# Optimization experiments

Hardware: AMD Instinct MI355X
Metric: run time of the kernel (lower is better)

Reference implementation:

```python
import jax, jax.numpy as jnp
import numpy as np

EMBED_DIM = 128
B, SQ, SKV = 16, 2048, 2048


def setup_inputs() -> dict:
    key = jax.random.key(0)
    ks = jax.random.split(key, 8)
    d = EMBED_DIM
    scale = 1.0 / np.sqrt(d)
    return {
        "x": jax.random.normal(ks[0], (B, SQ, d), dtype=jnp.float32),
        "y": jax.random.normal(ks[1], (B, SKV, d), dtype=jnp.float32),
        "Wq": jax.random.normal(ks[2], (d, d), dtype=jnp.float32) * scale,
        "bq": jax.random.normal(ks[3], (d,), dtype=jnp.float32) * 0.02,
        "Wk": jax.random.normal(ks[4], (d, d), dtype=jnp.float32) * scale,
        "bk": jax.random.normal(ks[5], (d,), dtype=jnp.float32) * 0.02,
        "Wv": jax.random.normal(ks[6], (d, d), dtype=jnp.float32) * scale,
        "bv": jax.random.normal(ks[7], (d,), dtype=jnp.float32) * 0.02,
    }


def reference(x, y, Wq, bq, Wk, bk, Wv, bv):
    # Linear projections (torch Linear: x @ W.T + b; here W stored as [in,out])
    q = x @ Wq + bq            # [B, SQ, d]
    k = y @ Wk + bk            # [B, SKV, d]
    v = y @ Wv + bv            # [B, SKV, d]
    # Source scales by q.size(-1)**0.5 = sqrt(embed_dim)
    inv_scale = 1.0 / jnp.sqrt(jnp.asarray(q.shape[-1], q.dtype))
    scores = jnp.einsum("bqd,bkd->bqk", q, k) * inv_scale  # [B, SQ, SKV]
    attn = jax.nn.softmax(scores, axis=-1)
    return jnp.einsum("bqk,bkd->bqd", attn, v)
```

## Files before the change

kernel.cpp:

```cpp
#include <hip/hip_runtime.h>
#include <hip/hip_bf16.h>

typedef unsigned short ushort_t;
typedef __attribute__((ext_vector_type(8))) short short8;
typedef __attribute__((ext_vector_type(4))) float f32x4;
typedef __attribute__((ext_vector_type(16))) float f32x16;

#define MFMA16(a, b, c) __builtin_amdgcn_mfma_f32_16x16x32_bf16((a), (b), (c), 0, 0, 0)
#define MFMA32(a, b, c) __builtin_amdgcn_mfma_f32_32x32x16_bf16((a), (b), (c), 0, 0, 0)

__device__ __forceinline__ ushort_t f2bf(float f) {
    return __builtin_bit_cast(ushort_t, __float2bfloat16(f));
}

#define CVTPK(lo, hi) ({ unsigned int r_; \
    asm("v_cvt_pk_bf16_f32 %0, %1, %2" : "=v"(r_) : "v"(lo), "v"(hi)); r_; })

__device__ __forceinline__ void gl_lds16(const void* g, void* l) {
    __builtin_amdgcn_global_load_lds((const __attribute__((address_space(1))) void*)g,
                                     (__attribute__((address_space(3))) void*)l, 16, 0, 0);
}

__global__ __launch_bounds__(256) void wt_kernel(
    const float* __restrict__ Wq, const float* __restrict__ Wk, const float* __restrict__ Wv,
    ushort_t* __restrict__ WTq, ushort_t* __restrict__ WTk, ushort_t* __restrict__ WTv)
{
    __shared__ __align__(16) ushort_t wt2[128 * 24];

    const int mat  = blockIdx.x >> 3;
    const int slab = blockIdx.x & 7;
    const float* W = (mat == 0) ? Wq : (mat == 1) ? Wk : Wv;
    ushort_t*   WT = (mat == 0) ? WTq : (mat == 1) ? WTk : WTv;

    const int t = threadIdx.x;
    #pragma unroll
    for (int i = 0; i < 2; ++i) {
        int idx = t + i * 256;
        int kloc = idx >> 5;
        int c0   = (idx & 31) * 4;
        f32x4 v = ((const f32x4*)(W + (size_t)(slab * 16) * 128))[idx];
        #pragma unroll
        for (int j = 0; j < 4; ++j)
            wt2[(c0 + j) * 24 + kloc] = f2bf(v[j]);
    }
    __syncthreads();
    const int r    = t >> 1;
    const int half = t & 1;
    short8 v8 = *(const short8*)&wt2[r * 24 + half * 8];
    *(short8*)(WT + r * 128 + slab * 16 + half * 8) = v8;
}

__global__ __launch_bounds__(256) void proj_kernel(
    const float* __restrict__ src, const ushort_t* __restrict__ WT,
    const float* __restrict__ bias, ushort_t* __restrict__ dst, float scale)
{
    const int t = threadIdx.x;
    const int w  = t >> 6;
    const int l  = t & 63;
    const int lg = l >> 4;
    const int ln = l & 15;
    const int r0 = blockIdx.x * 64 + w * 16;
    const int acol = lg * 8;

    short8 afrag[4];
    #pragma unroll
    for (int kc = 0; kc < 4; ++kc) {
        const f32x4* p = (const f32x4*)(src + (size_t)(r0 + ln) * 128 + acol + kc * 32);
        f32x4 a0 = p[0], a1 = p[1];
        short8 a;
        #pragma unroll
        for (int j = 0; j < 4; ++j) { a[j] = (short)f2bf(a0[j]); a[4 + j] = (short)f2bf(a1[j]); }
        afrag[kc] = a;
    }

    #pragma unroll
    for (int ct = 0; ct < 8; ++ct) {
        f32x4 acc = {0.f, 0.f, 0.f, 0.f};
        const int c = ct * 16 + ln;
        #pragma unroll
        for (int kc = 0; kc < 4; ++kc) {
            short8 bfr = *(const short8*)(WT + c * 128 + kc * 32 + acol);
            acc = MFMA16(afrag[kc], bfr, acc);
        }
        float bv = bias[c];
        #pragma unroll
        for (int reg = 0; reg < 4; ++reg) {
            int row = r0 + lg * 4 + reg;
            dst[(size_t)row * 128 + c] = f2bf((acc[reg] + bv) * scale);
        }
    }
}

__global__ __launch_bounds__(256) void projKV_kernel(
    const float* __restrict__ src,
    const ushort_t* __restrict__ WTk, const float* __restrict__ bk,
    const ushort_t* __restrict__ WTv, const float* __restrict__ bv,
    ushort_t* __restrict__ Kd, ushort_t* __restrict__ VTd)
{
    __shared__ __align__(16) ushort_t vt[128 * 64];

    const int t = threadIdx.x;
    const int w  = t >> 6;
    const int l  = t & 63;
    const int lg = l >> 4;
    const int ln = l & 15;
    const int r0 = blockIdx.x * 64 + w * 16;
    const int acol = lg * 8;

    short8 afrag[4];
    #pragma unroll
    for (int kc = 0; kc < 4; ++kc) {
        const f32x4* p = (const f32x4*)(src + (size_t)(r0 + ln) * 128 + acol + kc * 32);
        f32x4 a0 = p[0], a1 = p[1];
        short8 a;
        #pragma unroll
        for (int j = 0; j < 4; ++j) { a[j] = (short)f2bf(a0[j]); a[4 + j] = (short)f2bf(a1[j]); }
        afrag[kc] = a;
    }

    #pragma unroll
    for (int ct = 0; ct < 8; ++ct) {
        f32x4 acc = {0.f, 0.f, 0.f, 0.f};
        const int c = ct * 16 + ln;
        #pragma unroll
        for (int kc = 0; kc < 4; ++kc) {
            short8 bfr = *(const short8*)(WTk + c * 128 + kc * 32 + acol);
            acc = MFMA16(afrag[kc], bfr, acc);
        }
        float bvv = bk[c];
        #pragma unroll
        for (int reg = 0; reg < 4; ++reg) {
            int row = r0 + lg * 4 + reg;
            Kd[(size_t)row * 128 + c] = f2bf(acc[reg] + bvv);
        }
    }

    #pragma unroll
    for (int ct = 0; ct < 8; ++ct) {
        f32x4 acc = {0.f, 0.f, 0.f, 0.f};
        const int c = ct * 16 + ln;
        #pragma unroll
        for (int kc = 0; kc < 4; ++kc) {
            short8 bfr = *(const short8*)(WTv + c * 128 + kc * 32 + acol);
            acc = MFMA16(afrag[kc], bfr, acc);
        }
        float bvv = bv[c];
        #pragma unroll
        for (int reg = 0; reg < 4; ++reg) {
            int rloc = w * 16 + lg * 4 + reg;
            int byte = (c * 128 + rloc * 2) ^ ((c & 7) << 4);
            *(ushort_t*)((char*)vt + byte) = f2bf(acc[reg] + bvv);
        }
    }
    __syncthreads();

    const int r0b = blockIdx.x * 64;
    const int b   = r0b >> 11;
    const int kv0 = r0b & 2047;
    const int c    = t >> 1;
    const int half = t & 1;
    ushort_t* dst = VTd + (size_t)b * 128 * 2048 + (size_t)c * 2048 + kv0 + half * 32;
    #pragma unroll
    for (int j = 0; j < 4; ++j) {
        int byte = (c * 128 + (half * 32 + j * 8) * 2) ^ ((c & 7) << 4);
        *(short8*)(dst + j * 8) = *(const short8*)((const char*)vt + byte);
    }
}

#define KVBLK 64
#define NT (2048 / KVBLK)
__global__ __launch_bounds__(256) void attn_kernel(
    const ushort_t* __restrict__ Q, const ushort_t* __restrict__ K,
    const ushort_t* __restrict__ VT, float* __restrict__ out)
{
    __shared__ __align__(16) char smem_[65536];

    const int t = threadIdx.x;
    const int bid = (int)blockIdx.x;
    const int wg = (bid & 7) * 64 + (bid >> 3);
    const int b  = wg >> 5;
    const int q0blk = (wg & 31) * 64;

    const char* Kb  = (const char*)(K  + (size_t)b * 2048 * 128);
    const char* VTb = (const char*)(VT + (size_t)b * 128 * 2048);
    const ushort_t* Qb = Q + (size_t)b * 2048 * 128;

    const int w   = t >> 6;
    const int qg  = w >> 1;
    const int kvh = w & 1;
    const int l  = t & 63;
    const int lq = l & 31;
    const int h  = l >> 5;
    const int swz = (l & 7) << 4;
    const int q0 = q0blk + qg * 32;

    short8 qfrag[8];
    {
        const ushort_t* qp = Qb + (size_t)(q0 + lq) * 128 + h * 8;
        #pragma unroll
        for (int kc = 0; kc < 8; ++kc)
            qfrag[kc] = *(const short8*)(qp + kc * 16);
    }

    f32x16 o[4];
    #pragma unroll
    for (int db = 0; db < 4; ++db)
        #pragma unroll
        for (int i = 0; i < 16; ++i) o[db][i] = 0.f;
    float m = -__builtin_inff(), lsum = 0.f;

    auto stage = [&](int buf, int kt) {
        const char* kb = Kb + (size_t)kt * KVBLK * 256;
        const int kv2 = kt * KVBLK * 2;
        char* kd = smem_ + buf * 16384;
        char* vd = smem_ + 32768 + buf * 16384;
        #pragma unroll
        for (int i = 0; i < 4; ++i) {
            int base = w * 4096 + i * 1024;
            int p = base + l * 16;
            int spk = p ^ (((p >> 8) & 7) << 4);
            gl_lds16(kb + spk, kd + base);
            int spv = p ^ (((p >> 7) & 7) << 4);
            gl_lds16(VTb + (size_t)(spv >> 7) * 4096 + kv2 + (spv & 127), vd + base);
        }
    };

    stage(0, 0);
    int cur = 0;

    for (int kt = 0; kt < NT; ++kt) {
        __syncthreads();
        if (kt + 1 < NT) stage(cur ^ 1, kt + 1);

        const char* klp = smem_ + cur * 16384;
        f32x16 s;
        #pragma unroll
        for (int i = 0; i < 16; ++i) s[i] = 0.f;
        const int krow = kvh * 32 + lq;
        __builtin_amdgcn_s_setprio(1);
        #pragma unroll
        for (int kc = 0; kc < 8; ++kc) {
            int col = (h * 16 + kc * 32) ^ swz;
            short8 kf = *(const short8*)(klp + krow * 256 + col);
            s = MFMA32(kf, qfrag[kc], s);
        }
        __builtin_amdgcn_s_setprio(0);

        float mx;
        {
            float t8[8];
            #pragma unroll
            for (int i = 0; i < 8; ++i) t8[i] = fmaxf(s[i], s[i + 8]);
            #pragma unroll
            for (int i = 0; i < 4; ++i) t8[i] = fmaxf(t8[i], t8[i + 4]);
            mx = fmaxf(fmaxf(t8[0], t8[1]), fmaxf(t8[2], t8[3]));
        }
        mx = fmaxf(mx, __shfl_xor(mx, 32));

        if (__any(mx > m + 8.f)) {
            float mn = fmaxf(m, mx);
            float corr = __builtin_exp2f(m - mn);
            lsum *= corr;
            #pragma unroll
            for (int db = 0; db < 4; ++db)
                #pragma unroll
                for (int i = 0; i < 16; ++i) o[db][i] *= corr;
            m = mn;
        }
        #pragma unroll
        for (int i = 0; i < 16; ++i) s[i] = __builtin_exp2f(s[i] - m);
        float rs;
        {
            float a8[8];
            #pragma unroll
            for (int i = 0; i < 8; ++i) a8[i] = s[i] + s[i + 8];
            #pragma unroll
            for (int i = 0; i < 4; ++i) a8[i] += a8[i + 4];
            rs = (a8[0] + a8[1]) + (a8[2] + a8[3]);
        }
        rs += __shfl_xor(rs, 32);
        lsum += rs;

        short8 pf[2];
        {
            auto pack = [&](int a, short8& outf) {
                unsigned u0 = CVTPK(s[a * 8 + 0], s[a * 8 + 1]);
                unsigned u1 = CVTPK(s[a * 8 + 2], s[a * 8 + 3]);
                unsigned u2 = CVTPK(s[a * 8 + 4], s[a * 8 + 5]);
                unsigned u3 = CVTPK(s[a * 8 + 6], s[a * 8 + 7]);
                unsigned x0 = __shfl_xor(u0, 32);
                unsigned x1 = __shfl_xor(u1, 32);
                unsigned x2 = __shfl_xor(u2, 32);
                unsigned x3 = __shfl_xor(u3, 32);
                union { unsigned wds[4]; short8 s8; } f;
                f.wds[0] = h ? x2 : u0;
                f.wds[1] = h ? x3 : u1;
                f.wds[2] = h ? u2 : x0;
                f.wds[3] = h ? u3 : x1;
                outf = f.s8;
            };
            pack(0, pf[0]);
            pack(1, pf[1]);
        }

        const char* vlp = smem_ + 32768 + cur * 16384;
        __builtin_amdgcn_s_setprio(1);
        #pragma unroll
        for (int db = 0; db < 4; ++db) {
            int row = db * 32 + lq;
            #pragma unroll
            for (int ks = 0; ks < 2; ++ks) {
                int byte = row * 128 + ((kvh * 64 + ks * 32 + h * 16) ^ swz);
                short8 vf = *(const short8*)(vlp + byte);
                o[db] = MFMA32(vf, pf[ks], o[db]);
            }
        }
        __builtin_amdgcn_s_setprio(0);
        cur ^= 1;
    }

    __syncthreads();
    float* mrg = (float*)smem_;
    const int mo = qg * 4224 + lq * 132;
    const int mlb = 8448;

    if (kvh == 1) {
        #pragma unroll
        for (int db = 0; db < 4; ++db) {
            #pragma unroll
            for (int rq = 0; rq < 4; ++rq) {
                f32x4 v4;
                #pragma unroll
                for (int j = 0; j < 4; ++j) v4[j] = o[db][rq * 4 + j];
                *(f32x4*)&mrg[mo + db * 32 + rq * 8 + 4 * h] = v4;
            }
        }
        if (h == 0) {
            mrg[mlb + qg * 64 + lq] = m;
            mrg[mlb + 128 + qg * 64 + lq] = lsum;
        }
    }
    __syncthreads();
    if (kvh == 0) {
        float mB = mrg[mlb + qg * 64 + lq];
        float lB = mrg[mlb + 128 + qg * 64 + lq];
        float mF = fmaxf(m, mB);
        float cA = __builtin_exp2f(m - mF);
        float cB = __builtin_exp2f(mB - mF);
        float inv = 1.0f / (lsum * cA + lB * cB);
        float* ob = out + (size_t)b * 2048 * 128 + (size_t)(q0 + lq) * 128;
        #pragma unroll
        for (int db = 0; db < 4; ++db) {
            #pragma unroll
            for (int rq = 0; rq < 4; ++rq) {
                f32x4 p4 = *(const f32x4*)&mrg[mo + db * 32 + rq * 8 + 4 * h];
                f32x4 st;
                #pragma unroll
                for (int j = 0; j < 4; ++j)
                    st[j] = (o[db][rq * 4 + j] * cA + p4[j] * cB) * inv;
                *(f32x4*)(ob + db * 32 + rq * 8 + 4 * h) = st;
            }
        }
    }
}

extern "C" void kernel_launch(void* const* d_in, const int* in_sizes, int n_in,
                              void* d_out, int out_size, void* d_ws, size_t ws_size,
                              hipStream_t stream) {
    (void)in_sizes; (void)n_in; (void)out_size; (void)ws_size;
    const float* x  = (const float*)d_in[0];
    const float* y  = (const float*)d_in[1];
    const float* Wq = (const float*)d_in[2];
    const float* bq = (const float*)d_in[3];
    const float* Wk = (const float*)d_in[4];
    const float* bk = (const float*)d_in[5];
    const float* Wv = (const float*)d_in[6];
    const float* bv = (const float*)d_in[7];
    float* out = (float*)d_out;

    ushort_t* wtq = (ushort_t*)d_out;
    ushort_t* wtk = wtq + 16384;
    ushort_t* wtv = wtk + 16384;

    ushort_t* qws  = (ushort_t*)d_ws;
    ushort_t* kws  = qws + (size_t)32768 * 128;
    ushort_t* vtws = kws + (size_t)32768 * 128;

    const float qscale = (float)(1.4426950408889634 / 11.313708498984761);

    wt_kernel<<<24, 256, 0, stream>>>(Wq, Wk, Wv, wtq, wtk, wtv);
    proj_kernel<<<512, 256, 0, stream>>>(x, wtq, bq, qws, qscale);
    projKV_kernel<<<512, 256, 0, stream>>>(y, wtk, bk, wtv, bv, kws, vtws);
    attn_kernel<<<512, 256, 0, stream>>>(qws, kws, vtws, out);
}
```

Measured before the change: 103.4 us.

## Merge projection kernels and restructure attention to split KV across four waves

Q and KV projections are merged into one launch, and the Q/K outputs are staged through an LDS tile so global stores are coalesced. The attention kernel drops LDS double-buffered K/V staging in favour of direct global loads into registers. Each block now handles 32 queries, with the four waves splitting the KV range and combining their partial softmax states in a tree merge through LDS. Launch bounds request three blocks per CU. The aim is more parallelism and lower LDS pressure, at the cost of uncoalesced, unshared global K/V reads that rely on L2 and are repeated per block.

```diff
diff --git a/kernel.cpp b/kernel.cpp
--- a/kernel.cpp
+++ b/kernel.cpp
@@ -15,11 +15,6 @@
 
 #define CVTPK(lo, hi) ({ unsigned int r_; \
     asm("v_cvt_pk_bf16_f32 %0, %1, %2" : "=v"(r_) : "v"(lo), "v"(hi)); r_; })
-
-__device__ __forceinline__ void gl_lds16(const void* g, void* l) {
-    __builtin_amdgcn_global_load_lds((const __attribute__((address_space(1))) void*)g,
-                                     (__attribute__((address_space(3))) void*)l, 16, 0, 0);
-}
 
 __global__ __launch_bounds__(256) void wt_kernel(
     const float* __restrict__ Wq, const float* __restrict__ Wk, const float* __restrict__ Wv,
@@ -50,16 +45,27 @@
     *(short8*)(WT + r * 128 + slab * 16 + half * 8) = v8;
 }
 
-__global__ __launch_bounds__(256) void proj_kernel(
-    const float* __restrict__ src, const ushort_t* __restrict__ WT,
-    const float* __restrict__ bias, ushort_t* __restrict__ dst, float scale)
+__global__ __launch_bounds__(256) void proj_all(
+    const float* __restrict__ x, const float* __restrict__ y,
+    const ushort_t* __restrict__ WTq, const float* __restrict__ bq,
+    const ushort_t* __restrict__ WTk, const float* __restrict__ bk,
+    const ushort_t* __restrict__ WTv, const float* __restrict__ bv,
+    ushort_t* __restrict__ Qd, ushort_t* __restrict__ Kd, ushort_t* __restrict__ VTd,
+    float qscale)
 {
+    __shared__ __align__(16) ushort_t tile[64][140];
+    __shared__ __align__(16) ushort_t vt[128 * 64];
+
     const int t = threadIdx.x;
+    const bool isQ = blockIdx.x < 512;
+    const int pb = isQ ? blockIdx.x : (blockIdx.x - 512);
+    const float* src = isQ ? x : y;
+
     const int w  = t >> 6;
     const int l  = t & 63;
     const int lg = l >> 4;
     const int ln = l & 15;
-    const int r0 = blockIdx.x * 64 + w * 16;
+    const int r0 = pb * 64 + w * 16;
     const int acol = lg * 8;
 
     short8 afrag[4];
@@ -73,126 +79,89 @@
         afrag[kc] = a;
     }
 
+    const ushort_t* WT1 = isQ ? WTq : WTk;
+    const float*    b1  = isQ ? bq  : bk;
+    const float     sc  = isQ ? qscale : 1.0f;
+
     #pragma unroll
     for (int ct = 0; ct < 8; ++ct) {
         f32x4 acc = {0.f, 0.f, 0.f, 0.f};
         const int c = ct * 16 + ln;
         #pragma unroll
         for (int kc = 0; kc < 4; ++kc) {
-            short8 bfr = *(const short8*)(WT + c * 128 + kc * 32 + acol);
+            short8 bfr = *(const short8*)(WT1 + c * 128 + kc * 32 + acol);
             acc = MFMA16(afrag[kc], bfr, acc);
         }
-        float bv = bias[c];
-        #pragma unroll
-        for (int reg = 0; reg < 4; ++reg) {
-            int row = r0 + lg * 4 + reg;
-            dst[(size_t)row * 128 + c] = f2bf((acc[reg] + bv) * scale);
-        }
-    }
-}
-
-__global__ __launch_bounds__(256) void projKV_kernel(
-    const float* __restrict__ src,
-    const ushort_t* __restrict__ WTk, const float* __restrict__ bk,
-    const ushort_t* __restrict__ WTv, const float* __restrict__ bv,
-    ushort_t* __restrict__ Kd, ushort_t* __restrict__ VTd)
-{
-    __shared__ __align__(16) ushort_t vt[128 * 64];
-
-    const int t = threadIdx.x;
-    const int w  = t >> 6;
-    const int l  = t & 63;
-    const int lg = l >> 4;
-    const int ln = l & 15;
-    const int r0 = blockIdx.x * 64 + w * 16;
-    const int acol = lg * 8;
-
-    short8 afrag[4];
-    #pragma unroll
-    for (int kc = 0; kc < 4; ++kc) {
-        const f32x4* p = (const f32x4*)(src + (size_t)(r0 + ln) * 128 + acol + kc * 32);
-        f32x4 a0 = p[0], a1 = p[1];
-        short8 a;
-        #pragma unroll
-        for (int j = 0; j < 4; ++j) { a[j] = (short)f2bf(a0[j]); a[4 + j] = (short)f2bf(a1[j]); }
-        afrag[kc] = a;
-    }
-
-    #pragma unroll
-    for (int ct = 0; ct < 8; ++ct) {
-        f32x4 acc = {0.f, 0.f, 0.f, 0.f};
-        const int c = ct * 16 + ln;
-        #pragma unroll
-        for (int kc = 0; kc < 4; ++kc) {
-            short8 bfr = *(const short8*)(WTk + c * 128 + kc * 32 + acol);
-            acc = MFMA16(afrag[kc], bfr, acc);
-        }
-        float bvv = bk[c];
-        #pragma unroll
-        for (int reg = 0; reg < 4; ++reg) {
-            int row = r0 + lg * 4 + reg;
-            Kd[(size_t)row * 128 + c] = f2bf(acc[reg] + bvv);
-        }
-    }
-
-    #pragma unroll
-    for (int ct = 0; ct < 8; ++ct) {
-        f32x4 acc = {0.f, 0.f, 0.f, 0.f};
-        const int c = ct * 16 + ln;
-        #pragma unroll
-        for (int kc = 0; kc < 4; ++kc) {
-            short8 bfr = *(const short8*)(WTv + c * 128 + kc * 32 + acol);
-            acc = MFMA16(afrag[kc], bfr, acc);
-        }
-        float bvv = bv[c];
-        #pragma unroll
-        for (int reg = 0; reg < 4; ++reg) {
-            int rloc = w * 16 + lg * 4 + reg;
-            int byte = (c * 128 + rloc * 2) ^ ((c & 7) << 4);
-            *(ushort_t*)((char*)vt + byte) = f2bf(acc[reg] + bvv);
-        }
-    }
-    __syncthreads();
-
-    const int r0b = blockIdx.x * 64;
-    const int b   = r0b >> 11;
-    const int kv0 = r0b & 2047;
-    const int c    = t >> 1;
-    const int half = t & 1;
-    ushort_t* dst = VTd + (size_t)b * 128 * 2048 + (size_t)c * 2048 + kv0 + half * 32;
-    #pragma unroll
-    for (int j = 0; j < 4; ++j) {
-        int byte = (c * 128 + (half * 32 + j * 8) * 2) ^ ((c & 7) << 4);
-        *(short8*)(dst + j * 8) = *(const short8*)((const char*)vt + byte);
-    }
-}
-
-#define KVBLK 64
-#define NT (2048 / KVBLK)
-__global__ __launch_bounds__(256) void attn_kernel(
+        float bvv = b1[c];
+        #pragma unroll
+        for (int reg = 0; reg < 4; ++reg)
+            tile[w * 16 + lg * 4 + reg][c] = f2bf((acc[reg] + bvv) * sc);
+    }
+
+    if (!isQ) {
+        #pragma unroll
+        for (int ct = 0; ct < 8; ++ct) {
+            f32x4 acc = {0.f, 0.f, 0.f, 0.f};
+            const int c = ct * 16 + ln;
+            #pragma unroll
+            for (int kc = 0; kc < 4; ++kc) {
+                short8 bfr = *(const short8*)(WTv + c * 128 + kc * 32 + acol);
+                acc = MFMA16(afrag[kc], bfr, acc);
+            }
+            float bvv = bv[c];
+            #pragma unroll
+            for (int reg = 0; reg < 4; ++reg) {
+                int rloc = w * 16 + lg * 4 + reg;
+                int byte = (c * 128 + rloc * 2) ^ ((c & 7) << 4);
+                *(ushort_t*)((char*)vt + byte) = f2bf(acc[reg] + bvv);
+            }
+        }
+    }
+    __syncthreads();
+
+    {
+        const int row = t >> 2, ch = t & 3;
+        ushort_t* dst1 = (isQ ? Qd : Kd) + (size_t)(pb * 64 + row) * 128 + ch * 32;
+        #pragma unroll
+        for (int j = 0; j < 4; ++j)
+            *(short8*)(dst1 + j * 8) = *(const short8*)&tile[row][ch * 32 + j * 8];
+    }
+    if (!isQ) {
+        const int r0b = pb * 64;
+        const int b   = r0b >> 11;
+        const int kv0 = r0b & 2047;
+        const int c    = t >> 1;
+        const int half = t & 1;
+        ushort_t* dst = VTd + (size_t)b * 128 * 2048 + (size_t)c * 2048 + kv0 + half * 32;
+        #pragma unroll
+        for (int j = 0; j < 4; ++j) {
+            int byte = (c * 128 + (half * 32 + j * 8) * 2) ^ ((c & 7) << 4);
+            *(short8*)(dst + j * 8) = *(const short8*)((const char*)vt + byte);
+        }
+    }
+}
+
+__global__ __launch_bounds__(256, 3) void attn_kernel(
     const ushort_t* __restrict__ Q, const ushort_t* __restrict__ K,
     const ushort_t* __restrict__ VT, float* __restrict__ out)
 {
-    __shared__ __align__(16) char smem_[65536];
+    __shared__ float mrg[2][32][129];
+    __shared__ float mstat[2][2][32];
 
     const int t = threadIdx.x;
     const int bid = (int)blockIdx.x;
-    const int wg = (bid & 7) * 64 + (bid >> 3);
-    const int b  = wg >> 5;
-    const int q0blk = (wg & 31) * 64;
-
-    const char* Kb  = (const char*)(K  + (size_t)b * 2048 * 128);
-    const char* VTb = (const char*)(VT + (size_t)b * 128 * 2048);
-    const ushort_t* Qb = Q + (size_t)b * 2048 * 128;
-
-    const int w   = t >> 6;
-    const int qg  = w >> 1;
-    const int kvh = w & 1;
+    const int wg = (bid & 7) * 128 + (bid >> 3);
+    const int b  = wg >> 6;
+    const int q0 = (wg & 63) * 32;
+
+    const ushort_t* Qb  = Q  + (size_t)b * 2048 * 128;
+    const ushort_t* Kb  = K  + (size_t)b * 2048 * 128;
+    const ushort_t* VTb = VT + (size_t)b * 128 * 2048;
+
+    const int kvq = t >> 6;
     const int l  = t & 63;
     const int lq = l & 31;
     const int h  = l >> 5;
-    const int swz = (l & 7) << 4;
-    const int q0 = q0blk + qg * 32;
 
     short8 qfrag[8];
     {
@@ -209,42 +178,38 @@
         for (int i = 0; i < 16; ++i) o[db][i] = 0.f;
     float m = -__builtin_inff(), lsum = 0.f;
 
-    auto stage = [&](int buf, int kt) {
-        const char* kb = Kb + (size_t)kt * KVBLK * 256;
-        const int kv2 = kt * KVBLK * 2;
-        char* kd = smem_ + buf * 16384;
-        char* vd = smem_ + 32768 + buf * 16384;
-        #pragma unroll
-        for (int i = 0; i < 4; ++i) {
-            int base = w * 4096 + i * 1024;
-            int p = base + l * 16;
-            int spk = p ^ (((p >> 8) & 7) << 4);
-            gl_lds16(kb + spk, kd + base);
-            int spv = p ^ (((p >> 7) & 7) << 4);
-            gl_lds16(VTb + (size_t)(spv >> 7) * 4096 + kv2 + (spv & 127), vd + base);
-        }
-    };
-
-    stage(0, 0);
-    int cur = 0;
-
-    for (int kt = 0; kt < NT; ++kt) {
-        __syncthreads();
-        if (kt + 1 < NT) stage(cur ^ 1, kt + 1);
-
-        const char* klp = smem_ + cur * 16384;
+    for (int c = 0; c < 16; ++c) {
+        const int kbase = c * 128 + kvq * 32;
+
+        const ushort_t* kr = Kb + (size_t)(kbase + lq) * 128 + h * 8;
         f32x16 s;
         #pragma unroll
         for (int i = 0; i < 16; ++i) s[i] = 0.f;
-        const int krow = kvh * 32 + lq;
-        __builtin_amdgcn_s_setprio(1);
-        #pragma unroll
-        for (int kc = 0; kc < 8; ++kc) {
-            int col = (h * 16 + kc * 32) ^ swz;
-            short8 kf = *(const short8*)(klp + krow * 256 + col);
-            s = MFMA32(kf, qfrag[kc], s);
-        }
-        __builtin_amdgcn_s_setprio(0);
+        {
+            short8 kf[4];
+            #pragma unroll
+            for (int kc = 0; kc < 4; ++kc) kf[kc] = *(const short8*)(kr + kc * 16);
+            __builtin_amdgcn_s_setprio(1);
+            #pragma unroll
+            for (int kc = 0; kc < 4; ++kc) s = MFMA32(kf[kc], qfrag[kc], s);
+            __builtin_amdgcn_s_setprio(0);
+            #pragma unroll
+            for (int kc = 0; kc < 4; ++kc) kf[kc] = *(const short8*)(kr + 64 + kc * 16);
+            __builtin_amdgcn_s_setprio(1);
+            #pragma unroll
+            for (int kc = 0; kc < 4; ++kc) s = MFMA32(kf[kc], qfrag[4 + kc], s);
+            __builtin_amdgcn_s_setprio(0);
+        }
+
+        short8 vf[8];
+        {
+            const ushort_t* vr = VTb + (size_t)lq * 2048 + kbase + h * 8;
+            #pragma unroll
+            for (int db = 0; db < 4; ++db)
+                #pragma unroll
+                for (int ks = 0; ks < 2; ++ks)
+                    vf[db * 2 + ks] = *(const short8*)(vr + (size_t)db * 32 * 2048 + ks * 16);
+        }
 
         float mx;
         {
@@ -303,61 +268,62 @@
             pack(1, pf[1]);
         }
 
-        const char* vlp = smem_ + 32768 + cur * 16384;
         __builtin_amdgcn_s_setprio(1);
         #pragma unroll
         for (int db = 0; db < 4; ++db) {
-            int row = db * 32 + lq;
-            #pragma unroll
-            for (int ks = 0; ks < 2; ++ks) {
-                int byte = row * 128 + ((kvh * 64 + ks * 32 + h * 16) ^ swz);
-                short8 vf = *(const short8*)(vlp + byte);
-                o[db] = MFMA32(vf, pf[ks], o[db]);
-            }
+            #pragma unroll
+            for (int ks = 0; ks < 2; ++ks)
+                o[db] = MFMA32(vf[db * 2 + ks], pf[ks], o[db]);
         }
         __builtin_amdgcn_s_setprio(0);
-        cur ^= 1;
-    }
-
-    __syncthreads();
-    float* mrg = (float*)smem_;
-    const int mo = qg * 4224 + lq * 132;
-    const int mlb = 8448;
-
-    if (kvh == 1) {
-        #pragma unroll
-        for (int db = 0; db < 4; ++db) {
-            #pragma unroll
-            for (int rq = 0; rq < 4; ++rq) {
-                f32x4 v4;
-                #pragma unroll
-                for (int j = 0; j < 4; ++j) v4[j] = o[db][rq * 4 + j];
-                *(f32x4*)&mrg[mo + db * 32 + rq * 8 + 4 * h] = v4;
-            }
-        }
-        if (h == 0) {
-            mrg[mlb + qg * 64 + lq] = m;
-            mrg[mlb + 128 + qg * 64 + lq] = lsum;
-        }
-    }
-    __syncthreads();
-    if (kvh == 0) {
-        float mB = mrg[mlb + qg * 64 + lq];
-        float lB = mrg[mlb + 128 + qg * 64 + lq];
+    }
+
+    auto publish = [&](int slot) {
+        #pragma unroll
+        for (int db = 0; db < 4; ++db)
+            #pragma unroll
+            for (int i = 0; i < 16; ++i) {
+                int dr = db * 32 + (i & 3) + 8 * (i >> 2) + 4 * h;
+                mrg[slot][lq][dr] = o[db][i];
+            }
+        if (h == 0) { mstat[slot][0][lq] = m; mstat[slot][1][lq] = lsum; }
+    };
+    auto absorb = [&](int slot) {
+        float mB = mstat[slot][0][lq];
+        float lB = mstat[slot][1][lq];
         float mF = fmaxf(m, mB);
         float cA = __builtin_exp2f(m - mF);
         float cB = __builtin_exp2f(mB - mF);
-        float inv = 1.0f / (lsum * cA + lB * cB);
-        float* ob = out + (size_t)b * 2048 * 128 + (size_t)(q0 + lq) * 128;
+        lsum = lsum * cA + lB * cB;
+        m = mF;
+        #pragma unroll
+        for (int db = 0; db < 4; ++db)
+            #pragma unroll
+            for (int i = 0; i < 16; ++i) {
+                int dr = db * 32 + (i & 3) + 8 * (i >> 2) + 4 * h;
+                o[db][i] = o[db][i] * cA + mrg[slot][lq][dr] * cB;
+            }
+    };
+
+    if (kvq == 1) publish(0);
+    if (kvq == 3) publish(1);
+    __syncthreads();
+    if (kvq == 0) absorb(0);
+    if (kvq == 2) absorb(1);
+    __syncthreads();
+    if (kvq == 2) publish(0);
+    __syncthreads();
+    if (kvq == 0) {
+        absorb(0);
+        float inv = 1.0f / lsum;
+        float* ob = out + ((size_t)b * 2048 + q0 + lq) * 128;
         #pragma unroll
         for (int db = 0; db < 4; ++db) {
             #pragma unroll
             for (int rq = 0; rq < 4; ++rq) {
-                f32x4 p4 = *(const f32x4*)&mrg[mo + db * 32 + rq * 8 + 4 * h];
                 f32x4 st;
                 #pragma unroll
-                for (int j = 0; j < 4; ++j)
-                    st[j] = (o[db][rq * 4 + j] * cA + p4[j] * cB) * inv;
+                for (int j = 0; j < 4; ++j) st[j] = o[db][rq * 4 + j] * inv;
                 *(f32x4*)(ob + db * 32 + rq * 8 + 4 * h) = st;
             }
         }
@@ -389,7 +355,6 @@
     const float qscale = (float)(1.4426950408889634 / 11.313708498984761);
 
     wt_kernel<<<24, 256, 0, stream>>>(Wq, Wk, Wv, wtq, wtk, wtv);
-    proj_kernel<<<512, 256, 0, stream>>>(x, wtq, bq, qws, qscale);
-    projKV_kernel<<<512, 256, 0, stream>>>(y, wtk, bk, wtv, bv, kws, vtws);
-    attn_kernel<<<512, 256, 0, stream>>>(qws, kws, vtws, out);
-}
+    proj_all<<<1024, 256, 0, stream>>>(x, y, wtq, bq, wtk, bk, wtv, bv, qws, kws, vtws, qscale);
+    attn_kernel<<<1024, 256, 0, stream>>>(qws, kws, vtws, out);
+}
```

New measurement: 164.9 us. 1.6x slower.

## Merge Q and KV projections into one launch, row-sum via MFMA, max3 reductions

Applied to the files above, without the earlier changes.

Combines the Q and K/V projection kernels into a single 1024-block launch and stages Q/K outputs through LDS so they are written as coalesced 16-byte stores instead of scattered 2-byte stores. In the attention loop, the softmax row-sum is now accumulated with an MFMA against a ones vector instead of a scalar add tree plus a cross-lane shuffle. The row-max reduction uses v_max3_f32. These changes trade vector ALU work and shuffles for extra matrix-core work, and they add an extra 16-register accumulator that may raise register pressure.

```diff
diff --git a/kernel.cpp b/kernel.cpp
--- a/kernel.cpp
+++ b/kernel.cpp
@@ -15,6 +15,12 @@
 
 #define CVTPK(lo, hi) ({ unsigned int r_; \
     asm("v_cvt_pk_bf16_f32 %0, %1, %2" : "=v"(r_) : "v"(lo), "v"(hi)); r_; })
+
+__device__ __forceinline__ float max3f(float a, float b, float c) {
+    float d;
+    asm("v_max3_f32 %0, %1, %2, %3" : "=v"(d) : "v"(a), "v"(b), "v"(c));
+    return d;
+}
 
 __device__ __forceinline__ void gl_lds16(const void* g, void* l) {
     __builtin_amdgcn_global_load_lds((const __attribute__((address_space(1))) void*)g,
@@ -50,16 +56,27 @@
     *(short8*)(WT + r * 128 + slab * 16 + half * 8) = v8;
 }
 
-__global__ __launch_bounds__(256) void proj_kernel(
-    const float* __restrict__ src, const ushort_t* __restrict__ WT,
-    const float* __restrict__ bias, ushort_t* __restrict__ dst, float scale)
+__global__ __launch_bounds__(256) void proj_all(
+    const float* __restrict__ x, const float* __restrict__ y,
+    const ushort_t* __restrict__ WTq, const float* __restrict__ bq,
+    const ushort_t* __restrict__ WTk, const float* __restrict__ bk,
+    const ushort_t* __restrict__ WTv, const float* __restrict__ bv,
+    ushort_t* __restrict__ Qd, ushort_t* __restrict__ Kd, ushort_t* __restrict__ VTd,
+    float qscale)
 {
+    __shared__ __align__(16) ushort_t tile[64][140];
+    __shared__ __align__(16) ushort_t vt[128 * 64];
+
     const int t = threadIdx.x;
+    const bool isQ = blockIdx.x < 512;
+    const int pb = isQ ? blockIdx.x : (blockIdx.x - 512);
+    const float* src = isQ ? x : y;
+
     const int w  = t >> 6;
     const int l  = t & 63;
     const int lg = l >> 4;
     const int ln = l & 15;
-    const int r0 = blockIdx.x * 64 + w * 16;
+    const int r0 = pb * 64 + w * 16;
     const int acol = lg * 8;
 
     short8 afrag[4];
@@ -73,97 +90,65 @@
         afrag[kc] = a;
     }
 
+    const ushort_t* WT1 = isQ ? WTq : WTk;
+    const float*    b1  = isQ ? bq  : bk;
+    const float     sc  = isQ ? qscale : 1.0f;
+
     #pragma unroll
     for (int ct = 0; ct < 8; ++ct) {
         f32x4 acc = {0.f, 0.f, 0.f, 0.f};
         const int c = ct * 16 + ln;
         #pragma unroll
         for (int kc = 0; kc < 4; ++kc) {
-            short8 bfr = *(const short8*)(WT + c * 128 + kc * 32 + acol);
+            short8 bfr = *(const short8*)(WT1 + c * 128 + kc * 32 + acol);
             acc = MFMA16(afrag[kc], bfr, acc);
         }
-        float bv = bias[c];
-        #pragma unroll
-        for (int reg = 0; reg < 4; ++reg) {
-            int row = r0 + lg * 4 + reg;
-            dst[(size_t)row * 128 + c] = f2bf((acc[reg] + bv) * scale);
-        }
-    }
-}
-
-__global__ __launch_bounds__(256) void projKV_kernel(
-    const float* __restrict__ src,
-    const ushort_t* __restrict__ WTk, const float* __restrict__ bk,
-    const ushort_t* __restrict__ WTv, const float* __restrict__ bv,
-    ushort_t* __restrict__ Kd, ushort_t* __restrict__ VTd)
-{
-    __shared__ __align__(16) ushort_t vt[128 * 64];
-
-    const int t = threadIdx.x;
-    const int w  = t >> 6;
-    const int l  = t & 63;
-    const int lg = l >> 4;
-    const int ln = l & 15;
-    const int r0 = blockIdx.x * 64 + w * 16;
-    const int acol = lg * 8;
-
-    short8 afrag[4];
-    #pragma unroll
-    for (int kc = 0; kc < 4; ++kc) {
-        const f32x4* p = (const f32x4*)(src + (size_t)(r0 + ln) * 128 + acol + kc * 32);
-        f32x4 a0 = p[0], a1 = p[1];
-        short8 a;
-        #pragma unroll
-        for (int j = 0; j < 4; ++j) { a[j] = (short)f2bf(a0[j]); a[4 + j] = (short)f2bf(a1[j]); }
-        afrag[kc] = a;
-    }
-
-    #pragma unroll
-    for (int ct = 0; ct < 8; ++ct) {
-        f32x4 acc = {0.f, 0.f, 0.f, 0.f};
-        const int c = ct * 16 + ln;
-        #pragma unroll
-        for (int kc = 0; kc < 4; ++kc) {
-            short8 bfr = *(const short8*)(WTk + c * 128 + kc * 32 + acol);
-            acc = MFMA16(afrag[kc], bfr, acc);
-        }
-        float bvv = bk[c];
-        #pragma unroll
-        for (int reg = 0; reg < 4; ++reg) {
-            int row = r0 + lg * 4 + reg;
-            Kd[(size_t)row * 128 + c] = f2bf(acc[reg] + bvv);
-        }
-    }
-
-    #pragma unroll
-    for (int ct = 0; ct < 8; ++ct) {
-        f32x4 acc = {0.f, 0.f, 0.f, 0.f};
-        const int c = ct * 16 + ln;
-        #pragma unroll
-        for (int kc = 0; kc < 4; ++kc) {
-            short8 bfr = *(const short8*)(WTv + c * 128 + kc * 32 + acol);
-            acc = MFMA16(afrag[kc], bfr, acc);
-        }
-        float bvv = bv[c];
-        #pragma unroll
-        for (int reg = 0; reg < 4; ++reg) {
-            int rloc = w * 16 + lg * 4 + reg;
-            int byte = (c * 128 + rloc * 2) ^ ((c & 7) << 4);
-            *(ushort_t*)((char*)vt + byte) = f2bf(acc[reg] + bvv);
+        float bvv = b1[c];
+        #pragma unroll
+        for (int reg = 0; reg < 4; ++reg)
+            tile[w * 16 + lg * 4 + reg][c] = f2bf((acc[reg] + bvv) * sc);
+    }
+
+    if (!isQ) {
+        #pragma unroll
+        for (int ct = 0; ct < 8; ++ct) {
+            f32x4 acc = {0.f, 0.f, 0.f, 0.f};
+            const int c = ct * 16 + ln;
+            #pragma unroll
+            for (int kc = 0; kc < 4; ++kc) {
+                short8 bfr = *(const short8*)(WTv + c * 128 + kc * 32 + acol);
+                acc = MFMA16(afrag[kc], bfr, acc);
+            }
+            float bvv = bv[c];
+            #pragma unroll
+            for (int reg = 0; reg < 4; ++reg) {
+                int rloc = w * 16 + lg * 4 + reg;
+                int byte = (c * 128 + rloc * 2) ^ ((c & 7) << 4);
+                *(ushort_t*)((char*)vt + byte) = f2bf(acc[reg] + bvv);
+            }
         }
     }
     __syncthreads();
 
-    const int r0b = blockIdx.x * 64;
-    const int b   = r0b >> 11;
-    const int kv0 = r0b & 2047;
-    const int c    = t >> 1;
-    const int half = t & 1;
-    ushort_t* dst = VTd + (size_t)b * 128 * 2048 + (size_t)c * 2048 + kv0 + half * 32;
-    #pragma unroll
-    for (int j = 0; j < 4; ++j) {
-        int byte = (c * 128 + (half * 32 + j * 8) * 2) ^ ((c & 7) << 4);
-        *(short8*)(dst + j * 8) = *(const short8*)((const char*)vt + byte);
+    {
+        const int row = t >> 2, ch = t & 3;
+        ushort_t* dst1 = (isQ ? Qd : Kd) + (size_t)(pb * 64 + row) * 128 + ch * 32;
+        #pragma unroll
+        for (int j = 0; j < 4; ++j)
+            *(short8*)(dst1 + j * 8) = *(const short8*)&tile[row][ch * 32 + j * 8];
+    }
+    if (!isQ) {
+        const int r0b = pb * 64;
+        const int b   = r0b >> 11;
+        const int kv0 = r0b & 2047;
+        const int c    = t >> 1;
+        const int half = t & 1;
+        ushort_t* dst = VTd + (size_t)b * 128 * 2048 + (size_t)c * 2048 + kv0 + half * 32;
+        #pragma unroll
+        for (int j = 0; j < 4; ++j) {
+            int byte = (c * 128 + (half * 32 + j * 8) * 2) ^ ((c & 7) << 4);
+            *(short8*)(dst + j * 8) = *(const short8*)((const char*)vt + byte);
+        }
     }
 }
 
@@ -202,12 +187,19 @@
             qfrag[kc] = *(const short8*)(qp + kc * 16);
     }
 
+    short8 ones;
+    #pragma unroll
+    for (int i = 0; i < 8; ++i) ones[i] = (short)0x3F80;
+
     f32x16 o[4];
     #pragma unroll
     for (int db = 0; db < 4; ++db)
         #pragma unroll
         for (int i = 0; i < 16; ++i) o[db][i] = 0.f;
-    float m = -__builtin_inff(), lsum = 0.f;
+    f32x16 osum;
+    #pragma unroll
+    for (int i = 0; i < 16; ++i) osum[i] = 0.f;
+    float m = -__builtin_inff();
 
     auto stage = [&](int buf, int kt) {
         const char* kb = Kb + (size_t)kt * KVBLK * 256;
@@ -251,16 +243,17 @@
             float t8[8];
             #pragma unroll
             for (int i = 0; i < 8; ++i) t8[i] = fmaxf(s[i], s[i + 8]);
-            #pragma unroll
-            for (int i = 0; i < 4; ++i) t8[i] = fmaxf(t8[i], t8[i + 4]);
-            mx = fmaxf(fmaxf(t8[0], t8[1]), fmaxf(t8[2], t8[3]));
+            float m1 = max3f(t8[0], t8[1], t8[2]);
+            float m2 = max3f(t8[3], t8[4], t8[5]);
+            float m3 = max3f(t8[6], t8[7], m1);
+            mx = fmaxf(m2, m3);
         }
         mx = fmaxf(mx, __shfl_xor(mx, 32));
 
         if (__any(mx > m + 8.f)) {
             float mn = fmaxf(m, mx);
             float corr = __builtin_exp2f(m - mn);
-            lsum *= corr;
+            osum[0] *= corr;
             #pragma unroll
             for (int db = 0; db < 4; ++db)
                 #pragma unroll
@@ -269,17 +262,6 @@
         }
         #pragma unroll
         for (int i = 0; i < 16; ++i) s[i] = __builtin_exp2f(s[i] - m);
-        float rs;
-        {
-            float a8[8];
-            #pragma unroll
-            for (int i = 0; i < 8; ++i) a8[i] = s[i] + s[i + 8];
-            #pragma unroll
-            for (int i = 0; i < 4; ++i) a8[i] += a8[i + 4];
-            rs = (a8[0] + a8[1]) + (a8[2] + a8[3]);
-        }
-        rs += __shfl_xor(rs, 32);
-        lsum += rs;
 
         short8 pf[2];
         {
@@ -315,9 +297,13 @@
                 o[db] = MFMA32(vf, pf[ks], o[db]);
             }
         }
+        osum = MFMA32(ones, pf[0], osum);
+        osum = MFMA32(ones, pf[1], osum);
         __builtin_amdgcn_s_setprio(0);
         cur ^= 1;
     }
+
+    float lsum = osum[0];
 
     __syncthreads();
     float* mrg = (float*)smem_;
@@ -389,7 +375,6 @@
     const float qscale = (float)(1.4426950408889634 / 11.313708498984761);
 
     wt_kernel<<<24, 256, 0, stream>>>(Wq, Wk, Wv, wtq, wtk, wtv);
-    proj_kernel<<<512, 256, 0, stream>>>(x, wtq, bq, qws, qscale);
-    projKV_kernel<<<512, 256, 0, stream>>>(y, wtk, bk, wtv, bv, kws, vtws);
+    proj_all<<<1024, 256, 0, stream>>>(x, y, wtq, bq, wtk, bk, wtv, bv, qws, kws, vtws, qscale);
     attn_kernel<<<512, 256, 0, stream>>>(qws, kws, vtws, out);
 }
```

Result: slower. 128.0 us (+23.8%).
